# Performance work log

Measured on AMD Instinct MI355X. Metric: run time of the kernel, lower is better.

Reference implementation:

```python
import jax, jax.numpy as jnp
import numpy as np

K = 10
ALPHA = 0.1

def setup_inputs() -> dict:
    key = jax.random.key(0)
    k1, k2, k3, k4 = jax.random.split(key, 4)
    N, E, IN, HID, OUT = 100000, 3200000, 512, 256, 64
    x = jax.random.normal(k1, (N, IN), dtype=jnp.float32)
    edge_index = jax.random.randint(k2, (2, E), 0, N, dtype=jnp.int64)
    W1 = jax.random.normal(k3, (IN, HID), dtype=jnp.float32) * (1.0 / np.sqrt(IN))
    b1 = jnp.zeros((HID,), jnp.float32)
    W2 = jax.random.normal(k4, (HID, OUT), dtype=jnp.float32) * (1.0 / np.sqrt(HID))
    b2 = jnp.zeros((OUT,), jnp.float32)
    return {"x": x, "edge_index": edge_index, "W1": W1, "b1": b1, "W2": W2, "b2": b2}

def reference(x, edge_index, W1, b1, W2, b2):
    N = x.shape[0]
    # gcn_norm with self-loops (PyG default for APPNP)
    loop = jnp.arange(N, dtype=edge_index.dtype)
    src = jnp.concatenate([edge_index[0], loop])  # [E+N]
    dst = jnp.concatenate([edge_index[1], loop])
    ones = jnp.ones(src.shape[0], dtype=x.dtype)
    deg = jax.ops.segment_sum(ones, dst, num_segments=N)
    dis = jnp.where(deg > 0, jax.lax.rsqrt(deg), 0.0)
    norm = dis[src] * dis[dst]  # [E+N]

    # 2-layer MLP (dropout disabled: eval mode)
    h = jnp.maximum(x @ W1 + b1, 0.0) @ W2 + b2  # [N, out]

    # K-step PPR diffusion: z <- alpha*h + (1-alpha)*A_hat z
    def step(z, _):
        agg = jax.ops.segment_sum(norm[:, None] * z[src], dst, num_segments=N)
        return ALPHA * h + (1.0 - ALPHA) * agg, None

    z, _ = jax.lax.scan(step, h, None, length=K)
    return jax.nn.log_softmax(z, axis=-1)
```

## Files before the change

### kernel.cpp

```cpp
#include <hip/hip_runtime.h>
#include <hip/hip_bf16.h>

#define ALPHA_F 0.1f
#define KSTEPS 10
#define BKT_SH 9
#define P1_CHUNK 8192
#define MAXPAD_PER_BUCKET (512 * 32)

typedef __attribute__((ext_vector_type(8))) short bf16x8;
typedef __attribute__((ext_vector_type(4))) float f32x4;

__device__ __forceinline__ unsigned short f2bf(float f) {
  union { float f; unsigned int u; } v; v.f = f;
  unsigned int u = v.u;
  u += 0x7FFFu + ((u >> 16) & 1u);
  return (unsigned short)(u >> 16);
}
__device__ __forceinline__ float bflo(unsigned int u) { return __uint_as_float(u << 16); }
__device__ __forceinline__ float bfhi(unsigned int u) { return __uint_as_float(u & 0xFFFF0000u); }

__device__ __forceinline__ void gload16(const void* g, void* l) {
  __builtin_amdgcn_global_load_lds(
      (const __attribute__((address_space(1))) void*)g,
      (__attribute__((address_space(3))) void*)l, 16, 0, 0);
}


__global__ __launch_bounds__(256)
void p0_hist(const int* __restrict__ dstv, int E, int* __restrict__ bhist) {
  __shared__ int h[256];
  int t = threadIdx.x;
  h[t] = 0;
  __syncthreads();
  int b0 = blockIdx.x * P1_CHUNK;
  int lim = min(P1_CHUNK, E - b0);
  for (int i = t; i < lim; i += 256) atomicAdd(&h[dstv[b0 + i] >> BKT_SH], 1);
  __syncthreads();
  if (h[t]) atomicAdd(&bhist[t], h[t]);
}

__global__ void p0_scan(const int* __restrict__ bhist, int* __restrict__ bbase,
                        int* __restrict__ gcur) {
  __shared__ int s[256];
  int t = threadIdx.x;
  int mine = bhist[t];
  s[t] = mine;
  __syncthreads();
  for (int off = 1; off < 256; off <<= 1) {
    int v = (t >= off) ? s[t - off] : 0;
    __syncthreads();
    s[t] += v;
    __syncthreads();
  }
  int excl = s[t] - mine;
  bbase[t] = excl;
  gcur[t] = excl;
}

__global__ __launch_bounds__(256)
void p1_scatter(const int* __restrict__ srcv, const int* __restrict__ dstv, int E,
                int* __restrict__ gcur, int* __restrict__ tmp) {
  __shared__ int h[256];
  __shared__ int loc[256];
  int t = threadIdx.x;
  int b0 = blockIdx.x * P1_CHUNK;
  int lim = min(P1_CHUNK, E - b0);
  h[t] = 0;
  __syncthreads();
  for (int i = t; i < lim; i += 256) atomicAdd(&h[dstv[b0 + i] >> BKT_SH], 1);
  __syncthreads();
  loc[t] = h[t] ? atomicAdd(&gcur[t], h[t]) : 0;
  __syncthreads();
  h[t] = 0;
  __syncthreads();
  for (int i = t; i < lim; i += 256) {
    int d = dstv[b0 + i], s = srcv[b0 + i];
    int b = d >> BKT_SH;
    int pos = loc[b] + atomicAdd(&h[b], 1);
    tmp[pos] = (s << BKT_SH) | (d & 511);
  }
}

__global__ __launch_bounds__(256)
void p2_bucket(const int* __restrict__ tmp, const int* __restrict__ bbase,
               const int* __restrict__ bhist, int* __restrict__ counts,
               float* __restrict__ dis, int* __restrict__ rowptr,
               int* __restrict__ col, int N) {
  __shared__ int h1[512];
  __shared__ int cur[512];
  __shared__ int s2[256];
  const int t = threadIdx.x;
  const int b = blockIdx.x;
  const int base = bbase[b];
  const int pbase = base + b * MAXPAD_PER_BUCKET;
  const int sz = bhist[b];
  const int r0 = b << BKT_SH;
  const int nrows = min(512, N - r0);

  h1[t] = 0; h1[t + 256] = 0;
  __syncthreads();
  for (int i = t; i < sz; i += 256) atomicAdd(&h1[tmp[base + i] & 511], 1);
  __syncthreads();
  int a = (h1[2 * t] + 31) & ~31;
  int c = (h1[2 * t + 1] + 31) & ~31;
  s2[t] = a + c;
  __syncthreads();
  for (int off = 1; off < 256; off <<= 1) {
    int v = (t >= off) ? s2[t - off] : 0;
    __syncthreads();
    s2[t] += v;
    __syncthreads();
  }
  int excl2 = s2[t] - (a + c);
  cur[2 * t] = excl2;
  cur[2 * t + 1] = excl2 + a;
  __syncthreads();
  if (t < nrows) {
    rowptr[r0 + t] = pbase + cur[t];
    counts[r0 + t] = h1[t];
    dis[r0 + t] = rsqrtf((float)(h1[t] + 1));
  }
  if (t + 256 < nrows) {
    rowptr[r0 + t + 256] = pbase + cur[t + 256];
    counts[r0 + t + 256] = h1[t + 256];
    dis[r0 + t + 256] = rsqrtf((float)(h1[t + 256] + 1));
  }
  __syncthreads();
  for (int i = t; i < sz; i += 256) {
    int u = tmp[base + i];
    int p = pbase + atomicAdd(&cur[u & 511], 1);
    col[p] = u >> BKT_SH;
  }
  __syncthreads();
  for (int i = t; i < nrows; i += 256) {
    int cnt = h1[i];
    int c32 = (cnt + 31) & ~31;
    int ps = pbase + cur[i];
    for (int k = cnt; k < c32; ++k) col[ps++] = N;
  }
}

__global__ void k_zrow(unsigned short* __restrict__ yA, unsigned short* __restrict__ yB, int N) {
  int t = threadIdx.x;
  if (t < 64) yA[(size_t)N * 64 + t] = 0;
  else        yB[(size_t)N * 64 + (t - 64)] = 0;
}

__global__ void k_wconv1(const float* __restrict__ W, unsigned short* __restrict__ WT) {
  int idx = blockIdx.x * 256 + threadIdx.x;
  if (idx >= 512 * 256) return;
  int e = idx & 7, n = (idx >> 3) & 15, q = (idx >> 7) & 3;
  int nsub = (idx >> 9) & 15, kstep = idx >> 13;
  int k = kstep * 32 + q * 8 + e;
  int ncol = nsub * 16 + n;
  WT[idx] = f2bf(W[(size_t)k * 256 + ncol]);
}

__global__ void k_wconv2(const float* __restrict__ W, unsigned short* __restrict__ WT) {
  int idx = blockIdx.x * 256 + threadIdx.x;
  if (idx >= 256 * 64) return;
  int e = idx & 7, n = (idx >> 3) & 15, q = (idx >> 7) & 7;
  int nsub = (idx >> 10) & 3, kstep = idx >> 12;
  int k = kstep * 64 + q * 8 + e;
  int ncol = nsub * 16 + n;
  WT[idx] = f2bf(W[(size_t)k * 64 + ncol]);
}

__global__ __launch_bounds__(512)
void gemm1_kernel(const float* __restrict__ X, const unsigned short* __restrict__ Bt,
                  const float* __restrict__ bias, unsigned short* __restrict__ outT,
                  int M) {
  __shared__ __align__(16) unsigned short Al[2][4096];
  __shared__ __align__(16) unsigned short Bl[2][8192];
  const int t = threadIdx.x;
  const int m0 = blockIdx.x * 128;
  const int lane = t & 63;
  const int w = t >> 6;
  const int wm = w >> 2, wn = w & 3;

  const int am = t & 15;
  const int aq = (t >> 4) & 3;
  const int amsub = t >> 6;
  const int arow = m0 + amsub * 16 + am;
  const bool ag = arow < M;
  const int aoff = amsub * 512 + aq * 128 + am * 8;

  f32x4 acc[4][4] = {};

  {
    uint4 vv = {0, 0, 0, 0};
    if (ag) {
      const float* p = X + (size_t)arow * 512 + aq * 8;
      float4 a = *(const float4*)p, b = *(const float4*)(p + 4);
      unsigned short* o = (unsigned short*)&vv;
      o[0] = f2bf(a.x); o[1] = f2bf(a.y); o[2] = f2bf(a.z); o[3] = f2bf(a.w);
      o[4] = f2bf(b.x); o[5] = f2bf(b.y); o[6] = f2bf(b.z); o[7] = f2bf(b.w);
    }
    *(uint4*)&Al[0][aoff] = vv;
    gload16(Bt + (size_t)t * 8,         &Bl[0][t * 8]);
    gload16(Bt + (size_t)(t + 512) * 8, &Bl[0][(t + 512) * 8]);
  }
  __syncthreads();

  int cur = 0;
  for (int ks = 0; ks < 16; ++ks) {
    const bool more = ks < 15;
    float4 xa = {0, 0, 0, 0}, xb = {0, 0, 0, 0};
    if (more && ag) {
      const float* p = X + (size_t)arow * 512 + (ks + 1) * 32 + aq * 8;
      xa = *(const float4*)p;
      xb = *(const float4*)(p + 4);
    }
    bf16x8 af[4], bfv[4];
#pragma unroll
    for (int mi = 0; mi < 4; ++mi)
      af[mi] = *(const bf16x8*)&Al[cur][(((wm * 4 + mi) * 4 + (lane >> 4)) * 16 + (lane & 15)) * 8];
#pragma unroll
    for (int ni = 0; ni < 4; ++ni)
      bfv[ni] = *(const bf16x8*)&Bl[cur][(((wn * 4 + ni) * 4 + (lane >> 4)) * 16 + (lane & 15)) * 8];
#pragma unroll
    for (int mi = 0; mi < 4; ++mi)
#pragma unroll
      for (int ni = 0; ni < 4; ++ni)
        acc[mi][ni] = __builtin_amdgcn_mfma_f32_16x16x32_bf16(af[mi], bfv[ni], acc[mi][ni], 0, 0, 0);
    if (more) {
      uint4 vv = {0, 0, 0, 0};
      if (ag) {
        unsigned short* o = (unsigned short*)&vv;
        o[0] = f2bf(xa.x); o[1] = f2bf(xa.y); o[2] = f2bf(xa.z); o[3] = f2bf(xa.w);
        o[4] = f2bf(xb.x); o[5] = f2bf(xb.y); o[6] = f2bf(xb.z); o[7] = f2bf(xb.w);
      }
      *(uint4*)&Al[cur ^ 1][aoff] = vv;
      const unsigned short* bs = Bt + (size_t)(ks + 1) * 8192;
      gload16(bs + (size_t)t * 8,         &Bl[cur ^ 1][t * 8]);
      gload16(bs + (size_t)(t + 512) * 8, &Bl[cur ^ 1][(t + 512) * 8]);
    }
    __syncthreads();
    cur ^= 1;
  }

  unsigned short* ob = outT + (size_t)blockIdx.x * 32768;
#pragma unroll
  for (int mi = 0; mi < 4; ++mi) {
#pragma unroll
    for (int ni = 0; ni < 4; ++ni) {
      int n = wn * 64 + ni * 16 + (lane & 15);
      float bv = bias[n];
      int kstep = n >> 6, q = (n >> 3) & 7, e = n & 7;
#pragma unroll
      for (int j = 0; j < 4; ++j) {
        int lm = wm * 64 + mi * 16 + (lane >> 4) * 4 + j;
        if (m0 + lm < M) {
          float v = fmaxf(acc[mi][ni][j] + bv, 0.f);
          int msub = lm >> 4, mm = lm & 15;
          ob[((((kstep * 8 + msub) * 8 + q) * 16 + mm) * 8) + e] = f2bf(v);
        }
      }
    }
  }
}

__global__ __launch_bounds__(256)
void gemm2_kernel(const unsigned short* __restrict__ At, const unsigned short* __restrict__ Bt,
                  const float* __restrict__ bias, const float* __restrict__ dis,
                  unsigned short* __restrict__ hb, unsigned short* __restrict__ y0, int M) {
  __shared__ __align__(16) unsigned short Al[8192];
  __shared__ __align__(16) unsigned short Bl[4096];
  const int t = threadIdx.x;
  const int m0 = blockIdx.x * 128;
  const int lane = t & 63;
  const int w = t >> 6;
  const int wm = w >> 1, wn = w & 1;

  f32x4 acc[4][2] = {};

  const unsigned short* ab = At + (size_t)blockIdx.x * 32768;
  for (int ks = 0; ks < 4; ++ks) {
    const unsigned short* as = ab + ks * 8192;
    gload16(as + (size_t)t * 8,         &Al[t * 8]);
    gload16(as + (size_t)(t + 256) * 8, &Al[(t + 256) * 8]);
    gload16(as + (size_t)(t + 512) * 8, &Al[(t + 512) * 8]);
    gload16(as + (size_t)(t + 768) * 8, &Al[(t + 768) * 8]);
    const unsigned short* bs = Bt + ks * 4096;
    gload16(bs + (size_t)t * 8,         &Bl[t * 8]);
    gload16(bs + (size_t)(t + 256) * 8, &Bl[(t + 256) * 8]);
    __syncthreads();

#pragma unroll
    for (int kk = 0; kk < 2; ++kk) {
      bf16x8 af[4], bfv[2];
#pragma unroll
      for (int mi = 0; mi < 4; ++mi)
        af[mi] = *(const bf16x8*)&Al[((wm * 4 + mi) * 128 + kk * 64 + (lane >> 4) * 16 + (lane & 15)) * 8];
#pragma unroll
      for (int ni = 0; ni < 2; ++ni)
        bfv[ni] = *(const bf16x8*)&Bl[((wn * 2 + ni) * 128 + kk * 64 + (lane >> 4) * 16 + (lane & 15)) * 8];
#pragma unroll
      for (int mi = 0; mi < 4; ++mi)
#pragma unroll
        for (int ni = 0; ni < 2; ++ni)
          acc[mi][ni] = __builtin_amdgcn_mfma_f32_16x16x32_bf16(af[mi], bfv[ni], acc[mi][ni], 0, 0, 0);
    }
    __syncthreads();
  }

#pragma unroll
  for (int mi = 0; mi < 4; ++mi) {
#pragma unroll
    for (int ni = 0; ni < 2; ++ni) {
      int gn = wn * 32 + ni * 16 + (lane & 15);
      float bv = bias[gn];
#pragma unroll
      for (int j = 0; j < 4; ++j) {
        int gm = m0 + wm * 64 + mi * 16 + (lane >> 4) * 4 + j;
        if (gm < M) {
          float v = acc[mi][ni][j] + bv;
          hb[(size_t)gm * 64 + gn] = f2bf(v);
          y0[(size_t)gm * 64 + gn] = f2bf(dis[gm] * v);
        }
      }
    }
  }
}

template<bool FINAL>
__global__ __launch_bounds__(256)
void prop_kernel(const unsigned short* __restrict__ yin,
                 const unsigned short* __restrict__ hb,
                 void* __restrict__ yout,
                 const int* __restrict__ rowptr, const int* __restrict__ counts,
                 const int* __restrict__ col, const float* __restrict__ dis, int N) {
  int wid = (blockIdx.x * 256 + threadIdx.x) >> 6;
  wid = __builtin_amdgcn_readfirstlane(wid);
  if (wid >= N) return;
  const int lane = threadIdx.x & 63;
  const int g = lane >> 3;
  const int lg = lane & 7;
  const int r = wid;

  const int start = rowptr[r];
  const int cnt = counts[r];
  const int iters = (cnt + 31) >> 5;
  const float dr = dis[r];
  uint4 zs = *(const uint4*)(yin + (size_t)r * 64 + 8 * lg);
  uint4 hr = *(const uint4*)(hb + (size_t)r * 64 + 8 * lg);

  float acc[8] = {0.f, 0.f, 0.f, 0.f, 0.f, 0.f, 0.f, 0.f};
  const int* cp = col + start + 4 * g;
  for (int it = 0; it < iters; ++it, cp += 32) {
    int4 cc = *(const int4*)cp;
    uint4 z0 = *(const uint4*)(yin + (size_t)cc.x * 64 + 8 * lg);
    uint4 z1 = *(const uint4*)(yin + (size_t)cc.y * 64 + 8 * lg);
    uint4 z2 = *(const uint4*)(yin + (size_t)cc.z * 64 + 8 * lg);
    uint4 z3 = *(const uint4*)(yin + (size_t)cc.w * 64 + 8 * lg);
    acc[0] += bflo(z0.x); acc[1] += bfhi(z0.x); acc[2] += bflo(z0.y); acc[3] += bfhi(z0.y);
    acc[4] += bflo(z0.z); acc[5] += bfhi(z0.z); acc[6] += bflo(z0.w); acc[7] += bfhi(z0.w);
    acc[0] += bflo(z1.x); acc[1] += bfhi(z1.x); acc[2] += bflo(z1.y); acc[3] += bfhi(z1.y);
    acc[4] += bflo(z1.z); acc[5] += bfhi(z1.z); acc[6] += bflo(z1.w); acc[7] += bfhi(z1.w);
    acc[0] += bflo(z2.x); acc[1] += bfhi(z2.x); acc[2] += bflo(z2.y); acc[3] += bfhi(z2.y);
    acc[4] += bflo(z2.z); acc[5] += bfhi(z2.z); acc[6] += bflo(z2.w); acc[7] += bfhi(z2.w);
    acc[0] += bflo(z3.x); acc[1] += bfhi(z3.x); acc[2] += bflo(z3.y); acc[3] += bfhi(z3.y);
    acc[4] += bflo(z3.z); acc[5] += bfhi(z3.z); acc[6] += bflo(z3.w); acc[7] += bfhi(z3.w);
  }
#pragma unroll
  for (int k = 0; k < 8; ++k) {
    acc[k] += __shfl_xor(acc[k], 8);
    acc[k] += __shfl_xor(acc[k], 16);
    acc[k] += __shfl_xor(acc[k], 32);
  }

  float selfz[8] = { bflo(zs.x), bfhi(zs.x), bflo(zs.y), bfhi(zs.y),
                     bflo(zs.z), bfhi(zs.z), bflo(zs.w), bfhi(zs.w) };
  float hv[8]    = { bflo(hr.x), bfhi(hr.x), bflo(hr.y), bfhi(hr.y),
                     bflo(hr.z), bfhi(hr.z), bflo(hr.w), bfhi(hr.w) };
  float f[8];
#pragma unroll
  for (int k = 0; k < 8; ++k)
    f[k] = ALPHA_F * hv[k] + (1.f - ALPHA_F) * dr * (acc[k] + selfz[k]);

  if (!FINAL) {
    if (g == 0) {
      uint4 o;
      o.x = (unsigned)f2bf(dr * f[0]) | ((unsigned)f2bf(dr * f[1]) << 16);
      o.y = (unsigned)f2bf(dr * f[2]) | ((unsigned)f2bf(dr * f[3]) << 16);
      o.z = (unsigned)f2bf(dr * f[4]) | ((unsigned)f2bf(dr * f[5]) << 16);
      o.w = (unsigned)f2bf(dr * f[6]) | ((unsigned)f2bf(dr * f[7]) << 16);
      *(uint4*)((unsigned short*)yout + (size_t)r * 64 + 8 * lg) = o;
    }
  } else {
    float m = f[0];
#pragma unroll
    for (int k = 1; k < 8; ++k) m = fmaxf(m, f[k]);
    m = fmaxf(m, __shfl_xor(m, 1));
    m = fmaxf(m, __shfl_xor(m, 2));
    m = fmaxf(m, __shfl_xor(m, 4));
    float s = 0.f;
#pragma unroll
    for (int k = 0; k < 8; ++k) s += __expf(f[k] - m);
    s += __shfl_xor(s, 1);
    s += __shfl_xor(s, 2);
    s += __shfl_xor(s, 4);
    float ls = __logf(s);
    if (g == 0) {
      float* op = (float*)yout + (size_t)r * 64 + 8 * lg;
      *(float4*)op       = make_float4(f[0] - m - ls, f[1] - m - ls, f[2] - m - ls, f[3] - m - ls);
      *(float4*)(op + 4) = make_float4(f[4] - m - ls, f[5] - m - ls, f[6] - m - ls, f[7] - m - ls);
    }
  }
}

extern "C" void kernel_launch(void* const* d_in, const int* in_sizes, int n_in,
                              void* d_out, int out_size, void* d_ws, size_t ws_size,
                              hipStream_t stream) {
  const float* x  = (const float*)d_in[0];
  const int*   ei = (const int*)d_in[1];
  const float* W1 = (const float*)d_in[2];
  const float* b1 = (const float*)d_in[3];
  const float* W2 = (const float*)d_in[4];
  const float* b2 = (const float*)d_in[5];

  const int IN = 512, HID = 256, OUT = 64;
  const int N = in_sizes[0] / IN;
  const int E = in_sizes[1] / 2;
  const int* srcv = ei;
  const int* dstv = ei + E;
  const int NBUCK = (N + (1 << BKT_SH) - 1) >> BKT_SH;
  const int MT = (N + 127) / 128;
  const size_t N1 = (size_t)N + 1;

  char* p = (char*)d_ws;
  auto alloc = [&](size_t bytes) -> void* {
    void* r = (void*)p;
    p += (bytes + 255) & ~(size_t)255;
    return r;
  };
  int*   bhist  = (int*)alloc(256 * 4);
  int*   bbase  = (int*)alloc(256 * 4);
  int*   gcur   = (int*)alloc(256 * 4);
  int*   counts = (int*)alloc((size_t)N * 4);
  float* dis    = (float*)alloc((size_t)N * 4);
  int*   rowptr = (int*)alloc((size_t)N * 4);
  int*   col    = (int*)alloc(((size_t)E + 256 * MAXPAD_PER_BUCKET) * 4);
  unsigned short* WT1t = (unsigned short*)alloc((size_t)IN * HID * 2);
  unsigned short* WT2t = (unsigned short*)alloc((size_t)HID * OUT * 2);
  unsigned short* hb   = (unsigned short*)alloc((size_t)N * OUT * 2);
  unsigned short* yA   = (unsigned short*)alloc(N1 * OUT * 2);
  size_t hidT_bytes = (size_t)MT * 32768 * 2;
  size_t R_bytes = hidT_bytes;
  if ((size_t)E * 4 > R_bytes) R_bytes = (size_t)E * 4;
  if (N1 * OUT * 2 > R_bytes) R_bytes = N1 * OUT * 2;
  char* R = (char*)alloc(R_bytes);
  int* tmp = (int*)R;
  unsigned short* hidT = (unsigned short*)R;
  unsigned short* yB = (unsigned short*)R;

  hipMemsetAsync(bhist, 0, 256 * 4, stream);

  const int p1blocks = (E + P1_CHUNK - 1) / P1_CHUNK;
  p0_hist<<<p1blocks, 256, 0, stream>>>(dstv, E, bhist);
  p0_scan<<<1, 256, 0, stream>>>(bhist, bbase, gcur);
  p1_scatter<<<p1blocks, 256, 0, stream>>>(srcv, dstv, E, gcur, tmp);
  p2_bucket<<<NBUCK, 256, 0, stream>>>(tmp, bbase, bhist, counts, dis, rowptr, col, N);

  k_wconv1<<<(IN * HID + 255) / 256, 256, 0, stream>>>(W1, WT1t);
  k_wconv2<<<(HID * OUT + 255) / 256, 256, 0, stream>>>(W2, WT2t);

  gemm1_kernel<<<MT, 512, 0, stream>>>(x, WT1t, b1, hidT, N);
  gemm2_kernel<<<MT, 256, 0, stream>>>(hidT, WT2t, b2, dis, hb, yA, N);
  k_zrow<<<1, 128, 0, stream>>>(yA, yB, N);

  const int pblocks = (N + 3) / 4;
  const unsigned short* ycur = yA;
  for (int it = 0; it < KSTEPS - 1; ++it) {
    unsigned short* ynext = (it & 1) ? yA : yB;
    prop_kernel<false><<<pblocks, 256, 0, stream>>>(ycur, hb, ynext, rowptr, counts, col, dis, N);
    ycur = ynext;
  }
  prop_kernel<true><<<pblocks, 256, 0, stream>>>(ycur, hb, d_out, rowptr, counts, col, dis, N);
}
```

Baseline: 758.7 us.

## Drop LDS staging in gemm1, load MFMA operands directly from global memory

The first GEMM no longer stages X and W1 tiles through double-buffered shared memory with barriers. Each wave now loads its A fragments straight from fp32 X in global memory, converting to bf16 in registers, and reads its B fragments directly from the pre-swizzled weight buffer. This removes the LDS traffic and per-step __syncthreads. In exchange, global and L2 traffic rises because waves sharing rows or columns each reload them, and there is no explicit prefetch to overlap loads with MFMA.

```diff
diff --git a/kernel.cpp b/kernel.cpp
--- a/kernel.cpp
+++ b/kernel.cpp
@@ -170,73 +170,45 @@
 void gemm1_kernel(const float* __restrict__ X, const unsigned short* __restrict__ Bt,
                   const float* __restrict__ bias, unsigned short* __restrict__ outT,
                   int M) {
-  __shared__ __align__(16) unsigned short Al[2][4096];
-  __shared__ __align__(16) unsigned short Bl[2][8192];
   const int t = threadIdx.x;
-  const int m0 = blockIdx.x * 128;
   const int lane = t & 63;
   const int w = t >> 6;
   const int wm = w >> 2, wn = w & 3;
-
-  const int am = t & 15;
-  const int aq = (t >> 4) & 3;
-  const int amsub = t >> 6;
-  const int arow = m0 + amsub * 16 + am;
-  const bool ag = arow < M;
-  const int aoff = amsub * 512 + aq * 128 + am * 8;
+  const int m0 = blockIdx.x * 128;
+  const int mbase = m0 + wm * 64;
+  const int q = lane >> 4;
+  const int mr = lane & 15;
 
   f32x4 acc[4][4] = {};
 
-  {
-    uint4 vv = {0, 0, 0, 0};
-    if (ag) {
-      const float* p = X + (size_t)arow * 512 + aq * 8;
-      float4 a = *(const float4*)p, b = *(const float4*)(p + 4);
-      unsigned short* o = (unsigned short*)&vv;
+  const float* xr[4];
+#pragma unroll
+  for (int mi = 0; mi < 4; ++mi) {
+    int r = mbase + mi * 16 + mr;
+    if (r >= M) r = M - 1;
+    xr[mi] = X + (size_t)r * 512 + q * 8;
+  }
+  const unsigned short* bb = Bt + (((size_t)(wn * 4) * 4 + q) * 16 + mr) * 8;
+
+  for (int ks = 0; ks < 16; ++ks) {
+    bf16x8 af[4], bfv[4];
+#pragma unroll
+    for (int ni = 0; ni < 4; ++ni)
+      bfv[ni] = *(const bf16x8*)(bb + ((size_t)ks * 16 + ni) * 512);
+#pragma unroll
+    for (int mi = 0; mi < 4; ++mi) {
+      const float* p = xr[mi] + ks * 32;
+      float4 a = *(const float4*)p;
+      float4 b = *(const float4*)(p + 4);
+      unsigned short* o = (unsigned short*)&af[mi];
       o[0] = f2bf(a.x); o[1] = f2bf(a.y); o[2] = f2bf(a.z); o[3] = f2bf(a.w);
       o[4] = f2bf(b.x); o[5] = f2bf(b.y); o[6] = f2bf(b.z); o[7] = f2bf(b.w);
     }
-    *(uint4*)&Al[0][aoff] = vv;
-    gload16(Bt + (size_t)t * 8,         &Bl[0][t * 8]);
-    gload16(Bt + (size_t)(t + 512) * 8, &Bl[0][(t + 512) * 8]);
-  }
-  __syncthreads();
-
-  int cur = 0;
-  for (int ks = 0; ks < 16; ++ks) {
-    const bool more = ks < 15;
-    float4 xa = {0, 0, 0, 0}, xb = {0, 0, 0, 0};
-    if (more && ag) {
-      const float* p = X + (size_t)arow * 512 + (ks + 1) * 32 + aq * 8;
-      xa = *(const float4*)p;
-      xb = *(const float4*)(p + 4);
-    }
-    bf16x8 af[4], bfv[4];
-#pragma unroll
-    for (int mi = 0; mi < 4; ++mi)
-      af[mi] = *(const bf16x8*)&Al[cur][(((wm * 4 + mi) * 4 + (lane >> 4)) * 16 + (lane & 15)) * 8];
-#pragma unroll
-    for (int ni = 0; ni < 4; ++ni)
-      bfv[ni] = *(const bf16x8*)&Bl[cur][(((wn * 4 + ni) * 4 + (lane >> 4)) * 16 + (lane & 15)) * 8];
 #pragma unroll
     for (int mi = 0; mi < 4; ++mi)
 #pragma unroll
       for (int ni = 0; ni < 4; ++ni)
         acc[mi][ni] = __builtin_amdgcn_mfma_f32_16x16x32_bf16(af[mi], bfv[ni], acc[mi][ni], 0, 0, 0);
-    if (more) {
-      uint4 vv = {0, 0, 0, 0};
-      if (ag) {
-        unsigned short* o = (unsigned short*)&vv;
-        o[0] = f2bf(xa.x); o[1] = f2bf(xa.y); o[2] = f2bf(xa.z); o[3] = f2bf(xa.w);
-        o[4] = f2bf(xb.x); o[5] = f2bf(xb.y); o[6] = f2bf(xb.z); o[7] = f2bf(xb.w);
-      }
-      *(uint4*)&Al[cur ^ 1][aoff] = vv;
-      const unsigned short* bs = Bt + (size_t)(ks + 1) * 8192;
-      gload16(bs + (size_t)t * 8,         &Bl[cur ^ 1][t * 8]);
-      gload16(bs + (size_t)(t + 512) * 8, &Bl[cur ^ 1][(t + 512) * 8]);
-    }
-    __syncthreads();
-    cur ^= 1;
   }
 
   unsigned short* ob = outT + (size_t)blockIdx.x * 32768;
@@ -246,14 +218,14 @@
     for (int ni = 0; ni < 4; ++ni) {
       int n = wn * 64 + ni * 16 + (lane & 15);
       float bv = bias[n];
-      int kstep = n >> 6, q = (n >> 3) & 7, e = n & 7;
+      int kstep = n >> 6, qq = (n >> 3) & 7, e = n & 7;
 #pragma unroll
       for (int j = 0; j < 4; ++j) {
         int lm = wm * 64 + mi * 16 + (lane >> 4) * 4 + j;
         if (m0 + lm < M) {
           float v = fmaxf(acc[mi][ni][j] + bv, 0.f);
           int msub = lm >> 4, mm = lm & 15;
-          ob[((((kstep * 8 + msub) * 8 + q) * 16 + mm) * 8) + e] = f2bf(v);
+          ob[((((kstep * 8 + msub) * 8 + qq) * 16 + mm) * 8) + e] = f2bf(v);
         }
       }
     }
```

Result: slower. 854.3 us (+12.6%).

## Split gemm1 across two N-halves with 256-thread blocks and earlier prefetch

Applied to the files above, without the earlier changes.

Gemm1 now launches a 2D grid where each block computes a 128x128 output tile (half the hidden columns) with 256 threads instead of a 128x256 tile with 512 threads, halving B shared memory per block. The next-step B and X global loads are issued before the MFMA loop instead of after it, for more overlap. This doubles the number of blocks and reduces LDS per block, which may raise occupancy, but it means X is read from global memory and converted to bf16 twice.

```diff
diff --git a/kernel.cpp b/kernel.cpp
--- a/kernel.cpp
+++ b/kernel.cpp
@@ -166,50 +166,68 @@
   WT[idx] = f2bf(W[(size_t)k * 64 + ncol]);
 }
 
-__global__ __launch_bounds__(512)
+__global__ __launch_bounds__(256)
 void gemm1_kernel(const float* __restrict__ X, const unsigned short* __restrict__ Bt,
                   const float* __restrict__ bias, unsigned short* __restrict__ outT,
                   int M) {
   __shared__ __align__(16) unsigned short Al[2][4096];
-  __shared__ __align__(16) unsigned short Bl[2][8192];
+  __shared__ __align__(16) unsigned short Bl[2][4096];
   const int t = threadIdx.x;
   const int m0 = blockIdx.x * 128;
+  const int by = blockIdx.y;
   const int lane = t & 63;
   const int w = t >> 6;
-  const int wm = w >> 2, wn = w & 3;
-
-  const int am = t & 15;
-  const int aq = (t >> 4) & 3;
-  const int amsub = t >> 6;
-  const int arow = m0 + amsub * 16 + am;
-  const bool ag = arow < M;
-  const int aoff = amsub * 512 + aq * 128 + am * 8;
+  const int wm = w >> 1, wn = w & 1;
+
+  const int m_a = t & 15;
+  const int q_a = (t >> 4) & 3;
+  const int ms1 = t >> 6;
+  const int row1 = m0 + ms1 * 16 + m_a;
+  const int row2 = row1 + 64;
+  const bool g1 = row1 < M, g2 = row2 < M;
 
   f32x4 acc[4][4] = {};
 
   {
-    uint4 vv = {0, 0, 0, 0};
-    if (ag) {
-      const float* p = X + (size_t)arow * 512 + aq * 8;
+    uint4 v1 = {0, 0, 0, 0}, v2 = {0, 0, 0, 0};
+    if (g1) {
+      const float* p = X + (size_t)row1 * 512 + q_a * 8;
       float4 a = *(const float4*)p, b = *(const float4*)(p + 4);
-      unsigned short* o = (unsigned short*)&vv;
+      unsigned short* o = (unsigned short*)&v1;
       o[0] = f2bf(a.x); o[1] = f2bf(a.y); o[2] = f2bf(a.z); o[3] = f2bf(a.w);
       o[4] = f2bf(b.x); o[5] = f2bf(b.y); o[6] = f2bf(b.z); o[7] = f2bf(b.w);
     }
-    *(uint4*)&Al[0][aoff] = vv;
-    gload16(Bt + (size_t)t * 8,         &Bl[0][t * 8]);
-    gload16(Bt + (size_t)(t + 512) * 8, &Bl[0][(t + 512) * 8]);
+    if (g2) {
+      const float* p = X + (size_t)row2 * 512 + q_a * 8;
+      float4 a = *(const float4*)p, b = *(const float4*)(p + 4);
+      unsigned short* o = (unsigned short*)&v2;
+      o[0] = f2bf(a.x); o[1] = f2bf(a.y); o[2] = f2bf(a.z); o[3] = f2bf(a.w);
+      o[4] = f2bf(b.x); o[5] = f2bf(b.y); o[6] = f2bf(b.z); o[7] = f2bf(b.w);
+    }
+    *(uint4*)&Al[0][t * 8] = v1;
+    *(uint4*)&Al[0][(t + 256) * 8] = v2;
+    const unsigned short* bs = Bt + by * 4096;
+    gload16(bs + (size_t)t * 8,         &Bl[0][t * 8]);
+    gload16(bs + (size_t)(t + 256) * 8, &Bl[0][(t + 256) * 8]);
   }
   __syncthreads();
 
   int cur = 0;
   for (int ks = 0; ks < 16; ++ks) {
     const bool more = ks < 15;
-    float4 xa = {0, 0, 0, 0}, xb = {0, 0, 0, 0};
-    if (more && ag) {
-      const float* p = X + (size_t)arow * 512 + (ks + 1) * 32 + aq * 8;
-      xa = *(const float4*)p;
-      xb = *(const float4*)(p + 4);
+    float4 xa1 = {0,0,0,0}, xb1 = {0,0,0,0}, xa2 = {0,0,0,0}, xb2 = {0,0,0,0};
+    if (more) {
+      const unsigned short* bs = Bt + (size_t)(ks + 1) * 8192 + by * 4096;
+      gload16(bs + (size_t)t * 8,         &Bl[cur ^ 1][t * 8]);
+      gload16(bs + (size_t)(t + 256) * 8, &Bl[cur ^ 1][(t + 256) * 8]);
+      if (g1) {
+        const float* p = X + (size_t)row1 * 512 + (ks + 1) * 32 + q_a * 8;
+        xa1 = *(const float4*)p; xb1 = *(const float4*)(p + 4);
+      }
+      if (g2) {
+        const float* p = X + (size_t)row2 * 512 + (ks + 1) * 32 + q_a * 8;
+        xa2 = *(const float4*)p; xb2 = *(const float4*)(p + 4);
+      }
     }
     bf16x8 af[4], bfv[4];
 #pragma unroll
@@ -224,16 +242,19 @@
       for (int ni = 0; ni < 4; ++ni)
         acc[mi][ni] = __builtin_amdgcn_mfma_f32_16x16x32_bf16(af[mi], bfv[ni], acc[mi][ni], 0, 0, 0);
     if (more) {
-      uint4 vv = {0, 0, 0, 0};
-      if (ag) {
-        unsigned short* o = (unsigned short*)&vv;
-        o[0] = f2bf(xa.x); o[1] = f2bf(xa.y); o[2] = f2bf(xa.z); o[3] = f2bf(xa.w);
-        o[4] = f2bf(xb.x); o[5] = f2bf(xb.y); o[6] = f2bf(xb.z); o[7] = f2bf(xb.w);
+      uint4 v1 = {0, 0, 0, 0}, v2 = {0, 0, 0, 0};
+      if (g1) {
+        unsigned short* o = (unsigned short*)&v1;
+        o[0] = f2bf(xa1.x); o[1] = f2bf(xa1.y); o[2] = f2bf(xa1.z); o[3] = f2bf(xa1.w);
+        o[4] = f2bf(xb1.x); o[5] = f2bf(xb1.y); o[6] = f2bf(xb1.z); o[7] = f2bf(xb1.w);
       }
-      *(uint4*)&Al[cur ^ 1][aoff] = vv;
-      const unsigned short* bs = Bt + (size_t)(ks + 1) * 8192;
-      gload16(bs + (size_t)t * 8,         &Bl[cur ^ 1][t * 8]);
-      gload16(bs + (size_t)(t + 512) * 8, &Bl[cur ^ 1][(t + 512) * 8]);
+      if (g2) {
+        unsigned short* o = (unsigned short*)&v2;
+        o[0] = f2bf(xa2.x); o[1] = f2bf(xa2.y); o[2] = f2bf(xa2.z); o[3] = f2bf(xa2.w);
+        o[4] = f2bf(xb2.x); o[5] = f2bf(xb2.y); o[6] = f2bf(xb2.z); o[7] = f2bf(xb2.w);
+      }
+      *(uint4*)&Al[cur ^ 1][t * 8] = v1;
+      *(uint4*)&Al[cur ^ 1][(t + 256) * 8] = v2;
     }
     __syncthreads();
     cur ^= 1;
@@ -244,16 +265,16 @@
   for (int mi = 0; mi < 4; ++mi) {
 #pragma unroll
     for (int ni = 0; ni < 4; ++ni) {
-      int n = wn * 64 + ni * 16 + (lane & 15);
-      float bv = bias[n];
-      int kstep = n >> 6, q = (n >> 3) & 7, e = n & 7;
+      int gn = by * 128 + wn * 64 + ni * 16 + (lane & 15);
+      float bv = bias[gn];
+      int kstep = gn >> 6, qq = (gn >> 3) & 7, e = gn & 7;
 #pragma unroll
       for (int j = 0; j < 4; ++j) {
         int lm = wm * 64 + mi * 16 + (lane >> 4) * 4 + j;
         if (m0 + lm < M) {
           float v = fmaxf(acc[mi][ni][j] + bv, 0.f);
           int msub = lm >> 4, mm = lm & 15;
-          ob[((((kstep * 8 + msub) * 8 + q) * 16 + mm) * 8) + e] = f2bf(v);
+          ob[((((kstep * 8 + msub) * 8 + qq) * 16 + mm) * 8) + e] = f2bf(v);
         }
       }
     }
@@ -465,7 +486,8 @@
   k_wconv1<<<(IN * HID + 255) / 256, 256, 0, stream>>>(W1, WT1t);
   k_wconv2<<<(HID * OUT + 255) / 256, 256, 0, stream>>>(W2, WT2t);
 
-  gemm1_kernel<<<MT, 512, 0, stream>>>(x, WT1t, b1, hidT, N);
+  dim3 g1(MT, 2);
+  gemm1_kernel<<<g1, 256, 0, stream>>>(x, WT1t, b1, hidT, N);
   gemm2_kernel<<<MT, 256, 0, stream>>>(hidT, WT2t, b2, dis, hb, yA, N);
   k_zrow<<<1, 128, 0, stream>>>(yA, yB, N);
 
```

Result: slower. 789.9 us (+4.1%).
